# Performance work log

Hardware: AMD Instinct MI355X
Metric: run time of the kernel (lower is better)

## Reference

```python
import jax, jax.numpy as jnp
import numpy as np

D_MODEL = 1024
M = 4
NUM_EXPERTS = 8
TOP_K = 2
B, T = 2, 2048


def setup_inputs() -> dict:
    key = jax.random.key(0)
    ks = jax.random.split(key, 4)
    d_ff = D_MODEL * M
    x = jax.random.normal(ks[0], (B, T, D_MODEL), dtype=jnp.float32)
    # torch nn.Linear(d_model, num_experts, bias=False): stored here as (D, E) so logits = x @ gate_w
    gate_w = jax.random.normal(ks[1], (D_MODEL, NUM_EXPERTS), dtype=jnp.float32) * 0.02
    w1 = jax.random.normal(ks[2], (NUM_EXPERTS, D_MODEL, d_ff), dtype=jnp.float32) * 0.02
    b1 = jnp.zeros((NUM_EXPERTS, d_ff), dtype=jnp.float32)
    w2 = jax.random.normal(ks[3], (NUM_EXPERTS, d_ff, D_MODEL), dtype=jnp.float32) * 0.02
    b2 = jnp.zeros((NUM_EXPERTS, D_MODEL), dtype=jnp.float32)
    return {"x": x, "gate_w": gate_w, "w1": w1, "b1": b1, "w2": w2, "b2": b2}


def reference(x, gate_w, w1, b1, w2, b2):
    Bb, Tt, D = x.shape
    E = w1.shape[0]
    N = Bb * Tt
    # gating: top-k logits -> softmax over the k selected experts
    logits = jnp.einsum('btd,de->bte', x, gate_w)               # (B,T,E)
    top_v, top_i = jax.lax.top_k(logits, TOP_K)                 # (B,T,K)
    top_w = jax.nn.softmax(top_v, axis=-1)                      # (B,T,K)

    xf = x.reshape(N, D)
    idx = top_i.reshape(N, TOP_K)
    wts = top_w.reshape(N, TOP_K)
    # dense combine weights: comb[n, e] = sum_k wts[n,k] * [idx[n,k]==e]
    comb = jnp.zeros((N, E), dtype=x.dtype).at[jnp.arange(N)[:, None], idx].add(wts)

    # per-expert dense 2-layer MLP (exact erf GELU, matching torch F.gelu default),
    # combined with gate weights (zero weight == token not routed to expert).
    out = jnp.zeros((N, D), dtype=x.dtype)
    for e in range(E):
        h = jax.nn.gelu(xf @ w1[e] + b1[e], approximate=False)  # (N, D*M)
        out = out + comb[:, e:e + 1] * (h @ w2[e] + b2[e])      # (N, D)
    return out.reshape(Bb, Tt, D)
```

## Files before the change

### kernel.cpp

```cpp
#include <hip/hip_runtime.h>
#include <hip/hip_bf16.h>
#include <math.h>

#define D_MODEL 1024
#define D_FF    4096
#define NEXP    8
#define NTOK    4096
#define NROUTED 8192

typedef __attribute__((ext_vector_type(8))) short bf16x8;
typedef __attribute__((ext_vector_type(4))) float f32x4;
typedef __attribute__((ext_vector_type(4))) unsigned short us4;

#define WS_CNT   0
#define WS_CNT2  64
#define WS_OFF   128
#define WS_JOBS  192
#define WS_TI    512
#define WS_TW    (WS_TI + NTOK*2*4)
#define WS_TOK   (WS_TW + NTOK*2*4)
#define WS_GWT   (WS_TOK + NROUTED*4)
#define WS_XG    (((WS_GWT + NROUTED*4) + 255) & ~255)
#define WS_H     (WS_XG + (size_t)NROUTED*D_MODEL*2)
#define WS_WT    (WS_H + (size_t)NROUTED*D_FF*2)

__device__ __forceinline__ unsigned short f2bf(float f){
  union { float f; unsigned u; } a; a.f = f;
  unsigned u = a.u;
  u = u + 0x7FFF + ((u >> 16) & 1);
  return (unsigned short)(u >> 16);
}

__device__ __forceinline__ void gload_lds16(const void* g, void* l){
  __builtin_amdgcn_global_load_lds((const __attribute__((address_space(1))) void*)g,
                                   (__attribute__((address_space(3))) void*)l, 16, 0, 0);
}

__global__ void moe_gate_kernel(const float* __restrict__ x, const float* __restrict__ gw,
                                int* cnt, int* __restrict__ ti, float* __restrict__ tw){
  int n = blockIdx.x*4 + (threadIdx.x >> 6);
  int lane = threadIdx.x & 63;
  const float* xr = x + (size_t)n * D_MODEL;
  float acc[NEXP];
  #pragma unroll
  for (int e=0;e<NEXP;e++) acc[e] = 0.f;
  for (int d=lane; d<D_MODEL; d+=64){
    float xv = xr[d];
    #pragma unroll
    for (int e=0;e<NEXP;e++) acc[e] += xv * gw[d*NEXP + e];
  }
  #pragma unroll
  for (int e=0;e<NEXP;e++){
    #pragma unroll
    for (int o=32;o;o>>=1) acc[e] += __shfl_down(acc[e], o, 64);
  }
  if (lane == 0){
    int i0 = 0; float v0 = acc[0];
    #pragma unroll
    for (int e=1;e<NEXP;e++) if (acc[e] > v0){ v0 = acc[e]; i0 = e; }
    int i1 = -1; float v1 = -1e30f;
    #pragma unroll
    for (int e=0;e<NEXP;e++) if (e != i0 && acc[e] > v1){ v1 = acc[e]; i1 = e; }
    float p = expf(v1 - v0);
    float inv = 1.f / (1.f + p);
    ti[n*2] = i0; ti[n*2+1] = i1;
    tw[n*2] = inv; tw[n*2+1] = p * inv;
    atomicAdd(&cnt[i0], 1); atomicAdd(&cnt[i1], 1);
  }
}

__global__ void moe_prefix_kernel(const int* __restrict__ cnt, int* __restrict__ off,
                                  int* __restrict__ jobs){
  if (threadIdx.x == 0){
    int s = 0;
    for (int e=0;e<NEXP;e++){ off[e] = s; s += cnt[e]; }
    off[NEXP] = s;
    int idx = 0;
    for (int e=0;e<NEXP;e++){
      int ns = (cnt[e] + 127) >> 7;
      for (int q=0;q<ns;q++) jobs[1+idx++] = (e<<16) | q;
    }
    jobs[0] = idx;
  }
}

__global__ void moe_assign_kernel(const float* __restrict__ x, const int* __restrict__ ti,
                                  const float* __restrict__ tw, const int* __restrict__ off,
                                  int* cnt2, int* __restrict__ tok, float* __restrict__ gwt,
                                  unsigned short* __restrict__ Xg){
  __shared__ int ss[2];
  int n = blockIdx.x;
  if (threadIdx.x == 0){
    int i0 = ti[n*2], i1 = ti[n*2+1];
    int s0 = off[i0] + atomicAdd(&cnt2[i0], 1);
    int s1 = off[i1] + atomicAdd(&cnt2[i1], 1);
    tok[s0] = n; tok[s1] = n;
    gwt[s0] = tw[n*2]; gwt[s1] = tw[n*2+1];
    ss[0] = s0; ss[1] = s1;
  }
  __syncthreads();
  int s0 = ss[0], s1 = ss[1];
  int t = threadIdx.x;
  float4 v = ((const float4*)(x + (size_t)n * D_MODEL))[t];
  us4 pk = { f2bf(v.x), f2bf(v.y), f2bf(v.z), f2bf(v.w) };
  *(us4*)(Xg + (size_t)s0 * D_MODEL + t*4) = pk;
  *(us4*)(Xg + (size_t)s1 * D_MODEL + t*4) = pk;
}

__global__ __launch_bounds__(256) void transpose_bf16_kernel(
    const float* __restrict__ W, unsigned short* __restrict__ Wt, int K, int F){
  __shared__ float tile[64][65];
  int e = blockIdx.z;
  int f0 = blockIdx.x * 64, k0 = blockIdx.y * 64;
  const float* Wb = W + (size_t)e * K * F;
  unsigned short* Wtb = Wt + (size_t)e * F * K;
  int tid = threadIdx.x;
  #pragma unroll
  for (int i=0;i<4;i++){
    int idx = i*256 + tid;
    int r = idx >> 4, c4 = (idx & 15) * 4;
    float4 v = *(const float4*)(Wb + (size_t)(k0 + r) * F + f0 + c4);
    tile[r][c4] = v.x; tile[r][c4+1] = v.y; tile[r][c4+2] = v.z; tile[r][c4+3] = v.w;
  }
  __syncthreads();
  #pragma unroll
  for (int i=0;i<4;i++){
    int idx = i*256 + tid;
    int f = idx >> 4, k4 = (idx & 15) * 4;
    us4 pk = { f2bf(tile[k4][f]), f2bf(tile[k4+1][f]), f2bf(tile[k4+2][f]), f2bf(tile[k4+3][f]) };
    *(us4*)(Wtb + (size_t)(f0 + f) * K + k0 + k4) = pk;
  }
}

template<int MODE>
__global__ __launch_bounds__(512, 4) void moe_gemm_kernel(
    char* __restrict__ wsb, const unsigned short* __restrict__ Bt,
    const float* __restrict__ bias, float* __restrict__ out)
{
  const int* jobs = (const int*)(wsb + WS_JOBS);
  if ((int)blockIdx.y >= jobs[0]) return;
  const int jb = jobs[1 + blockIdx.y];
  const int e = jb >> 16;
  const int row0 = (jb & 0xffff) << 7;

  const int* off = (const int*)(wsb + WS_OFF);
  const int n0 = off[e];
  const int ne = off[e+1] - n0;

  constexpr int K = (MODE==1) ? D_MODEL : D_FF;
  const int bx     = (MODE==1) ? blockIdx.x : (blockIdx.x & 7);
  const int kchunk = (MODE==1) ? 0 : (blockIdx.x >> 3);
  const int n_off  = bx * 128;
  constexpr int nt = 16;
  const size_t kcb = (size_t)kchunk * 2048;

  const unsigned short* Ag  = (const unsigned short*)(wsb + (MODE==1 ? (size_t)WS_XG : (size_t)WS_H));
  const unsigned short* Bgt = Bt + (size_t)e * D_FF * D_MODEL;

  __shared__ __align__(16) char lds[2*32768];

  const int tid = threadIdx.x, lane = tid & 63, w = tid >> 6;
  const int wr = w >> 2, wc = w & 3;
  const int arow   = lane >> 3;
  const int achunk = ((lane & 7) ^ arow) << 4;

  const char* ptr_[4]; int doff_[4];
  #pragma unroll
  for (int i=0;i<4;i++){
    int c = w*4 + i;
    if (c < 16){
      int gr = row0 + c*8 + arow; if (gr >= ne) gr = ne - 1;
      ptr_[i]  = (const char*)(Ag + (size_t)(n0 + gr) * K) + kcb + achunk;
      doff_[i] = c*1024;
    } else {
      ptr_[i]  = (const char*)(Bgt + (size_t)(n_off + (c-16)*8 + arow) * K) + kcb + achunk;
      doff_[i] = 16384 + (c-16)*1024;
    }
  }

  f32x4 acc[4][2];
  #pragma unroll
  for (int i=0;i<4;i++)
    #pragma unroll
    for (int j=0;j<2;j++) acc[i][j] = (f32x4){0.f,0.f,0.f,0.f};

  #define STAGE(tt, ss) { \
    _Pragma("unroll") \
    for (int i=0;i<4;i++) \
      gload_lds16(ptr_[i] + (size_t)(tt)*128, lds + (ss)*32768 + doff_[i]); }

  STAGE(0, 0);
  asm volatile("s_waitcnt vmcnt(0)" ::: "memory");
  __builtin_amdgcn_s_barrier();

  int cur = 0;
  for (int t = 0; t < nt; ++t){
    if (t + 1 < nt) STAGE(t + 1, cur ^ 1);

    const char* base = lds + cur*32768;
    bf16x8 a[4][2], b[2][2];
    #pragma unroll
    for (int kk=0; kk<2; ++kk){
      #pragma unroll
      for (int mi=0; mi<4; mi++){
        int row = wr*64 + mi*16 + (lane&15);
        int byteoff = (row<<7) + (((kk<<6) + ((lane>>4)<<4)) ^ ((row&7)<<4));
        a[mi][kk] = *(const bf16x8*)(base + byteoff);
      }
      #pragma unroll
      for (int ni=0; ni<2; ni++){
        int col = wc*32 + ni*16 + (lane&15);
        int byteoff = 16384 + (col<<7) + (((kk<<6) + ((lane>>4)<<4)) ^ ((col&7)<<4));
        b[ni][kk] = *(const bf16x8*)(base + byteoff);
      }
    }
    asm volatile("s_waitcnt lgkmcnt(0)" ::: "memory");
    __builtin_amdgcn_sched_barrier(0);
    __builtin_amdgcn_s_setprio(1);
    #pragma unroll
    for (int kk=0; kk<2; ++kk)
      #pragma unroll
      for (int ni=0; ni<2; ni++)
        #pragma unroll
        for (int mi=0; mi<4; mi++)
          acc[mi][ni] = __builtin_amdgcn_mfma_f32_16x16x32_bf16(a[mi][kk], b[ni][kk], acc[mi][ni], 0, 0, 0);
    __builtin_amdgcn_s_setprio(0);
    __builtin_amdgcn_sched_barrier(0);
    asm volatile("s_waitcnt vmcnt(0)" ::: "memory");
    __builtin_amdgcn_s_barrier();
    cur ^= 1;
  }
  #undef STAGE

  if (MODE == 1){
    const float* b1 = bias + (size_t)e * D_FF;
    unsigned short* H = (unsigned short*)(wsb + (size_t)WS_H);
    #pragma unroll
    for (int mi=0; mi<4; mi++){
      int rbase = wr*64 + mi*16 + ((lane>>4)<<2);
      #pragma unroll
      for (int rr=0;rr<4;rr++){
        int lrow = rbase + rr;
        if (row0 + lrow < ne){
          size_t hb = (size_t)(n0 + row0 + lrow) * D_FF;
          #pragma unroll
          for (int ni=0; ni<2; ni++){
            int gcol = n_off + wc*32 + ni*16 + (lane&15);
            float v = acc[mi][ni][rr] + b1[gcol];
            v = 0.5f * v * (1.f + erff(v * 0.70710678118654752f));
            H[hb + gcol] = f2bf(v);
          }
        }
      }
    }
  } else {
    const float* b2 = bias + (size_t)e * D_MODEL;
    const int* tok = (const int*)(wsb + WS_TOK);
    const float* gwt = (const float*)(wsb + WS_GWT);
    #pragma unroll
    for (int mi=0; mi<4; mi++){
      int rbase = wr*64 + mi*16 + ((lane>>4)<<2);
      #pragma unroll
      for (int rr=0;rr<4;rr++){
        int lrow = rbase + rr;
        if (row0 + lrow < ne){
          int slot = n0 + row0 + lrow;
          int tk = tok[slot];
          float g = gwt[slot];
          float* orow = out + (size_t)tk * D_MODEL;
          #pragma unroll
          for (int ni=0; ni<2; ni++){
            int gcol = n_off + wc*32 + ni*16 + (lane&15);
            float bb = (kchunk == 0) ? b2[gcol] : 0.f;
            atomicAdd(orow + gcol, (acc[mi][ni][rr] + bb) * g);
          }
        }
      }
    }
  }
}

extern "C" void kernel_launch(void* const* d_in, const int* in_sizes, int n_in,
                              void* d_out, int out_size, void* d_ws, size_t ws_size,
                              hipStream_t stream){
  const float* x   = (const float*)d_in[0];
  const float* gw  = (const float*)d_in[1];
  const float* w1  = (const float*)d_in[2];
  const float* b1  = (const float*)d_in[3];
  const float* w2  = (const float*)d_in[4];
  const float* b2  = (const float*)d_in[5];
  float* out = (float*)d_out;
  char* ws = (char*)d_ws;
  unsigned short* Wt = (unsigned short*)(ws + (size_t)WS_WT);

  hipMemsetAsync(ws, 0, 512, stream);
  hipMemsetAsync(out, 0, (size_t)NTOK * D_MODEL * sizeof(float), stream);

  moe_gate_kernel<<<NTOK/4, 256, 0, stream>>>(x, gw, (int*)(ws+WS_CNT),
                                              (int*)(ws+WS_TI), (float*)(ws+WS_TW));
  moe_prefix_kernel<<<1, 64, 0, stream>>>((const int*)(ws+WS_CNT), (int*)(ws+WS_OFF),
                                          (int*)(ws+WS_JOBS));
  moe_assign_kernel<<<NTOK, 256, 0, stream>>>(x, (const int*)(ws+WS_TI),
                                              (const float*)(ws+WS_TW), (const int*)(ws+WS_OFF),
                                              (int*)(ws+WS_CNT2), (int*)(ws+WS_TOK),
                                              (float*)(ws+WS_GWT),
                                              (unsigned short*)(ws + (size_t)WS_XG));
  transpose_bf16_kernel<<<dim3(D_FF/64, D_MODEL/64, NEXP), 256, 0, stream>>>(w1, Wt, D_MODEL, D_FF);
  moe_gemm_kernel<1><<<dim3(D_FF/128, 71), 512, 0, stream>>>(ws, Wt, b1, out);
  transpose_bf16_kernel<<<dim3(D_MODEL/64, D_FF/64, NEXP), 256, 0, stream>>>(w2, Wt, D_FF, D_MODEL);
  moe_gemm_kernel<2><<<dim3((D_MODEL/128)*4, 71), 512, 0, stream>>>(ws, Wt, b2, out);
}
```

Baseline: 593.6 us.

## Enlarge grouped-GEMM tiles to 256x256 with 1024 threads and triple-buffered LDS

The routed-expert GEMM tile grows from 128x128 to 256x256 using 16 waves per block, with a K-step of 32 instead of 64. LDS becomes a three-stage ring that keeps two global-to-LDS loads in flight, synchronised with vmcnt waits, replacing the old double buffer. The job list is rebuilt with 256-row slices and the grid is capped at 40 jobs. Larger tiles give more reuse per loaded byte and fewer blocks. The cost is lower occupancy (one block per CU given 96KB LDS), more padding waste on partially filled expert slices, and a risk of dropped jobs if routing ever needs more than 40 slices.

```diff
diff --git a/kernel.cpp b/kernel.cpp
--- a/kernel.cpp
+++ b/kernel.cpp
@@ -7,6 +7,7 @@
 #define NEXP    8
 #define NTOK    4096
 #define NROUTED 8192
+#define MAXJOBS 40
 
 typedef __attribute__((ext_vector_type(8))) short bf16x8;
 typedef __attribute__((ext_vector_type(4))) float f32x4;
@@ -77,7 +78,7 @@
     off[NEXP] = s;
     int idx = 0;
     for (int e=0;e<NEXP;e++){
-      int ns = (cnt[e] + 127) >> 7;
+      int ns = (cnt[e] + 255) >> 8;
       for (int q=0;q<ns;q++) jobs[1+idx++] = (e<<16) | q;
     }
     jobs[0] = idx;
@@ -133,7 +134,7 @@
 }
 
 template<int MODE>
-__global__ __launch_bounds__(512, 4) void moe_gemm_kernel(
+__global__ __launch_bounds__(1024) void moe_gemm_kernel(
     char* __restrict__ wsb, const unsigned short* __restrict__ Bt,
     const float* __restrict__ bias, float* __restrict__ out)
 {
@@ -141,94 +142,85 @@
   if ((int)blockIdx.y >= jobs[0]) return;
   const int jb = jobs[1 + blockIdx.y];
   const int e = jb >> 16;
-  const int row0 = (jb & 0xffff) << 7;
+  const int row0 = (jb & 0xffff) << 8;
 
   const int* off = (const int*)(wsb + WS_OFF);
   const int n0 = off[e];
   const int ne = off[e+1] - n0;
 
-  constexpr int K = (MODE==1) ? D_MODEL : D_FF;
-  const int bx     = (MODE==1) ? blockIdx.x : (blockIdx.x & 7);
-  const int kchunk = (MODE==1) ? 0 : (blockIdx.x >> 3);
-  const int n_off  = bx * 128;
-  constexpr int nt = 16;
+  constexpr int K  = (MODE==1) ? D_MODEL : D_FF;
+  constexpr int NT = 32;
+  const int bx     = (MODE==1) ? blockIdx.x : (blockIdx.x & 3);
+  const int kchunk = (MODE==1) ? 0 : (blockIdx.x >> 2);
+  const int n_off  = bx * 256;
   const size_t kcb = (size_t)kchunk * 2048;
 
   const unsigned short* Ag  = (const unsigned short*)(wsb + (MODE==1 ? (size_t)WS_XG : (size_t)WS_H));
   const unsigned short* Bgt = Bt + (size_t)e * D_FF * D_MODEL;
 
-  __shared__ __align__(16) char lds[2*32768];
+  __shared__ __align__(16) char lds[3*32768];
 
   const int tid = threadIdx.x, lane = tid & 63, w = tid >> 6;
   const int wr = w >> 2, wc = w & 3;
-  const int arow   = lane >> 3;
-  const int achunk = ((lane & 7) ^ arow) << 4;
-
-  const char* ptr_[4]; int doff_[4];
-  #pragma unroll
-  for (int i=0;i<4;i++){
-    int c = w*4 + i;
-    if (c < 16){
-      int gr = row0 + c*8 + arow; if (gr >= ne) gr = ne - 1;
-      ptr_[i]  = (const char*)(Ag + (size_t)(n0 + gr) * K) + kcb + achunk;
-      doff_[i] = c*1024;
-    } else {
-      ptr_[i]  = (const char*)(Bgt + (size_t)(n_off + (c-16)*8 + arow) * K) + kcb + achunk;
-      doff_[i] = 16384 + (c-16)*1024;
-    }
-  }
-
-  f32x4 acc[4][2];
+
+  const int rA   = w*16 + (lane >> 2);
+  const int qs   = ((lane & 3) ^ ((rA >> 1) & 3)) << 4;
+  int grA = row0 + rA; if (grA >= ne) grA = ne - 1;
+  const char* aSrc = (const char*)(Ag + (size_t)(n0 + grA) * K) + kcb + qs;
+  const char* bSrc = (const char*)(Bgt + (size_t)(n_off + rA) * K) + kcb + qs;
+  const int dA = w*1024, dB = 16384 + w*1024;
+
+  const int q0 = lane >> 4;
+  int aoff[4], boff[4];
+  #pragma unroll
+  for (int mi=0; mi<4; mi++){
+    int row = wr*64 + mi*16 + (lane & 15);
+    aoff[mi] = row*64 + ((q0 ^ ((row>>1)&3)) << 4);
+  }
+  #pragma unroll
+  for (int ni=0; ni<4; ni++){
+    int col = wc*64 + ni*16 + (lane & 15);
+    boff[ni] = 16384 + col*64 + ((q0 ^ ((col>>1)&3)) << 4);
+  }
+
+  f32x4 acc[4][4];
   #pragma unroll
   for (int i=0;i<4;i++)
     #pragma unroll
-    for (int j=0;j<2;j++) acc[i][j] = (f32x4){0.f,0.f,0.f,0.f};
+    for (int j=0;j<4;j++) acc[i][j] = (f32x4){0.f,0.f,0.f,0.f};
 
   #define STAGE(tt, ss) { \
-    _Pragma("unroll") \
-    for (int i=0;i<4;i++) \
-      gload_lds16(ptr_[i] + (size_t)(tt)*128, lds + (ss)*32768 + doff_[i]); }
+    gload_lds16(aSrc + (size_t)(tt)*64, lds + (ss)*32768 + dA); \
+    gload_lds16(bSrc + (size_t)(tt)*64, lds + (ss)*32768 + dB); }
 
   STAGE(0, 0);
-  asm volatile("s_waitcnt vmcnt(0)" ::: "memory");
-  __builtin_amdgcn_s_barrier();
-
-  int cur = 0;
-  for (int t = 0; t < nt; ++t){
-    if (t + 1 < nt) STAGE(t + 1, cur ^ 1);
-
-    const char* base = lds + cur*32768;
-    bf16x8 a[4][2], b[2][2];
-    #pragma unroll
-    for (int kk=0; kk<2; ++kk){
-      #pragma unroll
-      for (int mi=0; mi<4; mi++){
-        int row = wr*64 + mi*16 + (lane&15);
-        int byteoff = (row<<7) + (((kk<<6) + ((lane>>4)<<4)) ^ ((row&7)<<4));
-        a[mi][kk] = *(const bf16x8*)(base + byteoff);
-      }
-      #pragma unroll
-      for (int ni=0; ni<2; ni++){
-        int col = wc*32 + ni*16 + (lane&15);
-        int byteoff = 16384 + (col<<7) + (((kk<<6) + ((lane>>4)<<4)) ^ ((col&7)<<4));
-        b[ni][kk] = *(const bf16x8*)(base + byteoff);
-      }
-    }
+  STAGE(1, 1);
+
+  for (int t = 0; t < NT; ++t){
+    if (t < NT-1) asm volatile("s_waitcnt vmcnt(2)" ::: "memory");
+    else          asm volatile("s_waitcnt vmcnt(0)" ::: "memory");
+    __builtin_amdgcn_s_barrier();
+    __builtin_amdgcn_sched_barrier(0);
+
+    if (t + 2 < NT) STAGE(t + 2, (t + 2) % 3);
+
+    const char* base = lds + (t % 3) * 32768;
+    bf16x8 a[4], b[4];
+    #pragma unroll
+    for (int mi=0; mi<4; mi++) a[mi] = *(const bf16x8*)(base + aoff[mi]);
+    #pragma unroll
+    for (int ni=0; ni<4; ni++) b[ni] = *(const bf16x8*)(base + boff[ni]);
+
     asm volatile("s_waitcnt lgkmcnt(0)" ::: "memory");
     __builtin_amdgcn_sched_barrier(0);
     __builtin_amdgcn_s_setprio(1);
     #pragma unroll
-    for (int kk=0; kk<2; ++kk)
+    for (int ni=0; ni<4; ni++)
       #pragma unroll
-      for (int ni=0; ni<2; ni++)
-        #pragma unroll
-        for (int mi=0; mi<4; mi++)
-          acc[mi][ni] = __builtin_amdgcn_mfma_f32_16x16x32_bf16(a[mi][kk], b[ni][kk], acc[mi][ni], 0, 0, 0);
+      for (int mi=0; mi<4; mi++)
+        acc[mi][ni] = __builtin_amdgcn_mfma_f32_16x16x32_bf16(a[mi], b[ni], acc[mi][ni], 0, 0, 0);
     __builtin_amdgcn_s_setprio(0);
     __builtin_amdgcn_sched_barrier(0);
-    asm volatile("s_waitcnt vmcnt(0)" ::: "memory");
-    __builtin_amdgcn_s_barrier();
-    cur ^= 1;
   }
   #undef STAGE
 
@@ -244,8 +236,8 @@
         if (row0 + lrow < ne){
           size_t hb = (size_t)(n0 + row0 + lrow) * D_FF;
           #pragma unroll
-          for (int ni=0; ni<2; ni++){
-            int gcol = n_off + wc*32 + ni*16 + (lane&15);
+          for (int ni=0; ni<4; ni++){
+            int gcol = n_off + wc*64 + ni*16 + (lane&15);
             float v = acc[mi][ni][rr] + b1[gcol];
             v = 0.5f * v * (1.f + erff(v * 0.70710678118654752f));
             H[hb + gcol] = f2bf(v);
@@ -269,8 +261,8 @@
           float g = gwt[slot];
           float* orow = out + (size_t)tk * D_MODEL;
           #pragma unroll
-          for (int ni=0; ni<2; ni++){
-            int gcol = n_off + wc*32 + ni*16 + (lane&15);
+          for (int ni=0; ni<4; ni++){
+            int gcol = n_off + wc*64 + ni*16 + (lane&15);
             float bb = (kchunk == 0) ? b2[gcol] : 0.f;
             atomicAdd(orow + gcol, (acc[mi][ni][rr] + bb) * g);
           }
@@ -306,7 +298,7 @@
                                               (float*)(ws+WS_GWT),
                                               (unsigned short*)(ws + (size_t)WS_XG));
   transpose_bf16_kernel<<<dim3(D_FF/64, D_MODEL/64, NEXP), 256, 0, stream>>>(w1, Wt, D_MODEL, D_FF);
-  moe_gemm_kernel<1><<<dim3(D_FF/128, 71), 512, 0, stream>>>(ws, Wt, b1, out);
+  moe_gemm_kernel<1><<<dim3(D_FF/256, MAXJOBS), 1024, 0, stream>>>(ws, Wt, b1, out);
   transpose_bf16_kernel<<<dim3(D_MODEL/64, D_FF/64, NEXP), 256, 0, stream>>>(w2, Wt, D_FF, D_MODEL);
-  moe_gemm_kernel<2><<<dim3((D_MODEL/128)*4, 71), 512, 0, stream>>>(ws, Wt, b2, out);
-}
+  moe_gemm_kernel<2><<<dim3((D_MODEL/256)*4, MAXJOBS), 1024, 0, stream>>>(ws, Wt, b2, out);
+}
```

After: 593.1 us. About the same (-0.1%).
